# Performance work log

Measured on AMD Instinct MI355X. Metric: run time of the kernel, lower is better.

## Reference

```python
import jax, jax.numpy as jnp
import numpy as np

NBIT = 4          # weight bit-width
GROUP_SIZE = 128  # weight quantization group size (divides k)
HAS_WEIGHT_ZEROS = True


def _quant_dequant_weights(w, group_size=GROUP_SIZE, nbit=NBIT, has_zeros=HAS_WEIGHT_ZEROS):
    # Mirrors torchao _quantize + quantize_per_channel_group, then dequantizes
    # (the native kernel dequantizes inline with the matmul; math is identical).
    qmin = -(1 << (nbit - 1))
    qmax = (1 << (nbit - 1)) - 1
    n, k = w.shape
    g = w.reshape(-1, group_size)                      # [n*k/gs, gs]
    vmin = g.min(axis=1, keepdims=True)
    vmax = g.max(axis=1, keepdims=True)
    scales = (vmax - vmin) / (qmax - qmin)             # per-group scale
    if has_zeros:
        zeros = qmin - jnp.round(vmin / scales)
    else:
        zeros = jnp.zeros_like(scales)
    q = jnp.clip(jnp.round(g / scales) + zeros, qmin, qmax)
    deq = (q - zeros) * scales
    return deq.reshape(n, k)


def _dyn_quant_dequant_act(x):
    # Dynamic per-token (per-row) asymmetric int8 activation quantization.
    qmin, qmax = -128, 127
    xmin = x.min(axis=-1, keepdims=True)
    xmax = x.max(axis=-1, keepdims=True)
    scale = (xmax - xmin) / (qmax - qmin)
    zero = qmin - jnp.round(xmin / scale)
    q = jnp.clip(jnp.round(x / scale) + zero, qmin, qmax)
    return (q - zero) * scale


def setup_inputs() -> dict:
    key = jax.random.key(0)
    k1, k2 = jax.random.split(key)
    x = jax.random.normal(k1, (4, 2048, 4096), dtype=jnp.float32)
    weights = jax.random.normal(k2, (4096, 4096), dtype=jnp.float32) * 0.02
    return {"x": x, "weights": weights}


def reference(x, weights):
    w_deq = _quant_dequant_weights(weights)            # [n, k]
    x_deq = _dyn_quant_dequant_act(x)                  # [..., m, k]
    # y[..., m, n] = x_deq @ w_deq^T
    return jnp.einsum('bmk,nk->bmn', x_deq, w_deq)
```

## Files before the change

kernel.cpp:

```cpp
#include <hip/hip_runtime.h>
#include <hip/hip_bf16.h>
#include <cfloat>

typedef __attribute__((ext_vector_type(8))) short bf16x8;
typedef __attribute__((ext_vector_type(4))) float f32x4;

#define M_DIM 8192
#define N_DIM 4096
#define K_DIM 4096

__device__ inline ushort f2bf(float f) {
    unsigned u = __float_as_uint(f);
    unsigned r = (u + 0x7FFFu + ((u >> 16) & 1u)) >> 16;
    return (ushort)r;
}

#define SWZ(x) ((x) ^ ((((x) >> 7) & 7) << 4))

__global__ __launch_bounds__(256) void w_dequant(const float* __restrict__ w,
                                                 ushort* __restrict__ wq) {
    int g = blockIdx.x * 4 + (threadIdx.x >> 6);
    int lane = threadIdx.x & 63;
    const float* src = w + (size_t)g * 128;
    float2 v = *(const float2*)(src + lane * 2);
    float mn = fminf(v.x, v.y), mx = fmaxf(v.x, v.y);
#pragma unroll
    for (int s = 1; s < 64; s <<= 1) {
        mn = fminf(mn, __shfl_xor(mn, s));
        mx = fmaxf(mx, __shfl_xor(mx, s));
    }
    float scale = (mx - mn) / 15.0f;
    float zero  = -8.0f - rintf(mn / scale);
    float q0 = fminf(fmaxf(rintf(v.x / scale) + zero, -8.0f), 7.0f);
    float q1 = fminf(fmaxf(rintf(v.y / scale) + zero, -8.0f), 7.0f);
    ushort2 o;
    o.x = f2bf((q0 - zero) * scale);
    o.y = f2bf((q1 - zero) * scale);
    *(ushort2*)(wq + (size_t)g * 128 + lane * 2) = o;
}

__global__ __launch_bounds__(256) void act_qdq(const float* __restrict__ x,
                                               ushort* __restrict__ xq) {
    __shared__ float smn[4], smx[4];
    int row = blockIdx.x;
    const float* xr = x + (size_t)row * K_DIM;
    ushort* xo = xq + (size_t)row * K_DIM;
    int t = threadIdx.x;
    float4 v[4];
    float mn = FLT_MAX, mx = -FLT_MAX;
#pragma unroll
    for (int i = 0; i < 4; i++) {
        v[i] = ((const float4*)xr)[t + i * 256];
        mn = fminf(mn, fminf(fminf(v[i].x, v[i].y), fminf(v[i].z, v[i].w)));
        mx = fmaxf(mx, fmaxf(fmaxf(v[i].x, v[i].y), fmaxf(v[i].z, v[i].w)));
    }
#pragma unroll
    for (int s = 1; s < 64; s <<= 1) {
        mn = fminf(mn, __shfl_xor(mn, s));
        mx = fmaxf(mx, __shfl_xor(mx, s));
    }
    int w = t >> 6;
    if ((t & 63) == 0) { smn[w] = mn; smx[w] = mx; }
    __syncthreads();
    mn = fminf(fminf(smn[0], smn[1]), fminf(smn[2], smn[3]));
    mx = fmaxf(fmaxf(smx[0], smx[1]), fmaxf(smx[2], smx[3]));
    float scale = (mx - mn) / 255.0f;
    float zero  = -128.0f - rintf(mn / scale);
#pragma unroll
    for (int i = 0; i < 4; i++) {
        float e0 = v[i].x, e1 = v[i].y, e2 = v[i].z, e3 = v[i].w;
        ushort4 o;
        float q;
        q = fminf(fmaxf(rintf(e0 / scale) + zero, -128.0f), 127.0f); o.x = f2bf((q - zero) * scale);
        q = fminf(fmaxf(rintf(e1 / scale) + zero, -128.0f), 127.0f); o.y = f2bf((q - zero) * scale);
        q = fminf(fmaxf(rintf(e2 / scale) + zero, -128.0f), 127.0f); o.z = f2bf((q - zero) * scale);
        q = fminf(fmaxf(rintf(e3 / scale) + zero, -128.0f), 127.0f); o.w = f2bf((q - zero) * scale);
        ((ushort4*)xo)[t + i * 256] = o;
    }
}

#define BM 256
#define BN 256
#define BK 64
#define NT (K_DIM / BK)

__global__ __launch_bounds__(512, 1) void gemm_bt8(const ushort* __restrict__ A,
                                                   const ushort* __restrict__ B,
                                                   float* __restrict__ C) {
    __shared__ __align__(16) ushort As[2][BM * BK];
    __shared__ __align__(16) ushort Bs[2][BN * BK];

    const int nbx = N_DIM / BN;
    const int nwg = (M_DIM / BM) * nbx;
    int bid = blockIdx.x;
    bid = (bid & 7) * (nwg / 8) + (bid >> 3);
    int mb = bid / nbx, nb = bid % nbx;
    size_t m0 = (size_t)mb * BM, n0 = (size_t)nb * BN;

    const int t = threadIdx.x;
    const int w = t >> 6, lane = t & 63;
    const int wm = w >> 2, wn = w & 3;
    const int lr = lane & 15;
    const int lk = (lane >> 4) << 3;

    const ushort* Ab = A + m0 * K_DIM;
    const ushort* Bb = B + n0 * K_DIM;

    auto STAGE = [&](int T, int qq) {
        if (T >= NT) return;
        int d = T & 1;
        bool isA = qq < 4;
        int rq = isA ? qq : qq - 4;
        ushort* reg = isA ? As[d] : Bs[d];
        const ushort* gbase = isA ? Ab : Bb;
        int base = rq * 8192 + w * 1024;
        int lb = base + lane * 16;
        int lg = SWZ(lb);
        int r = lg >> 7;
        int c = (lg & 127) >> 1;
        __builtin_amdgcn_global_load_lds(
            (const __attribute__((address_space(1))) unsigned int*)(gbase + (size_t)r * K_DIM + T * BK + c),
            (__attribute__((address_space(3))) unsigned int*)((char*)reg + base),
            16, 0, 0);
    };

    f32x4 acc[8][4] = {};
    bf16x8 afr[2][2][2];
    bf16x8 bfr[2][4][2];

#define LOADA(S, d, q) do {                                                       \
    _Pragma("unroll") for (int ii = 0; ii < 2; ii++)                              \
    _Pragma("unroll") for (int kk = 0; kk < 2; kk++) {                            \
        int row = (q) * 64 + wm * 32 + ii * 16 + lr;                              \
        int lg = row * 128 + (kk * 32 + lk) * 2;                                  \
        afr[S][ii][kk] = *(const bf16x8*)((const char*)As[d] + SWZ(lg));          \
    } } while (0)
#define LOADB(S, d) do {                                                          \
    _Pragma("unroll") for (int ni = 0; ni < 4; ni++)                              \
    _Pragma("unroll") for (int kk = 0; kk < 2; kk++) {                            \
        int row = wn * 64 + ni * 16 + lr;                                         \
        int lg = row * 128 + (kk * 32 + lk) * 2;                                  \
        bfr[S][ni][kk] = *(const bf16x8*)((const char*)Bs[d] + SWZ(lg));          \
    } } while (0)

#define PHASE(q, SA, SB, SN, dn, qn, sT1, sq1, sT2, sq2, vm) do {                 \
    __builtin_amdgcn_s_setprio(1);                                                \
    _Pragma("unroll") for (int kk = 0; kk < 2; kk++)                              \
    _Pragma("unroll") for (int ii = 0; ii < 2; ii++)                              \
    _Pragma("unroll") for (int ni = 0; ni < 4; ni++)                              \
        acc[(q) * 2 + ii][ni] = __builtin_amdgcn_mfma_f32_16x16x32_bf16(          \
            afr[SA][ii][kk], bfr[SB][ni][kk], acc[(q) * 2 + ii][ni], 0, 0, 0);    \
    __builtin_amdgcn_s_setprio(0);                                                \
    if ((qn) == 0) LOADB(dn, dn);                                                 \
    LOADA(SN, dn, qn);                                                            \
    STAGE(sT1, sq1);                                                              \
    STAGE(sT2, sq2);                                                              \
    asm volatile("s_waitcnt lgkmcnt(0)" ::: "memory");                            \
    if ((vm) == 0) asm volatile("s_waitcnt vmcnt(6)" ::: "memory");               \
    if ((vm) == 1) asm volatile("s_waitcnt vmcnt(2)" ::: "memory");               \
    if ((vm) == 2) asm volatile("s_waitcnt vmcnt(0)" ::: "memory");               \
    __builtin_amdgcn_s_barrier();                                                 \
    __builtin_amdgcn_sched_barrier(0);                                            \
  } while (0)

    STAGE(0, 0); STAGE(0, 1); STAGE(0, 2); STAGE(0, 3);
    STAGE(0, 4); STAGE(0, 5); STAGE(0, 6); STAGE(0, 7);
    STAGE(1, 4); STAGE(1, 5); STAGE(1, 6); STAGE(1, 7);
    STAGE(1, 0); STAGE(1, 1);
    asm volatile("s_waitcnt vmcnt(6)" ::: "memory");
    __builtin_amdgcn_s_barrier();
    LOADB(0, 0);
    LOADA(0, 0, 0);
    asm volatile("s_waitcnt lgkmcnt(0)" ::: "memory");
    __builtin_amdgcn_sched_barrier(0);

#pragma unroll 1
    for (int i = 0; i < NT / 2 - 1; i++) {
        int T0 = 2 * i;
        PHASE(0, 0, 0, 1, 0, 1, T0 + 1, 2, T0 + 1, 3, 0);
        PHASE(1, 1, 0, 0, 0, 2, T0 + 2, 4, T0 + 2, 5, 0);
        PHASE(2, 0, 0, 1, 0, 3, T0 + 2, 6, T0 + 2, 7, 0);
        PHASE(3, 1, 0, 0, 1, 0, T0 + 2, 0, T0 + 2, 1, 0);
        PHASE(0, 0, 1, 1, 1, 1, T0 + 2, 2, T0 + 2, 3, 0);
        PHASE(1, 1, 1, 0, 1, 2, T0 + 3, 4, T0 + 3, 5, 0);
        PHASE(2, 0, 1, 1, 1, 3, T0 + 3, 6, T0 + 3, 7, 0);
        PHASE(3, 1, 1, 0, 0, 0, T0 + 3, 0, T0 + 3, 1, 0);
    }

    PHASE(0, 0, 0, 1, 0, 1, NT - 1, 2, NT - 1, 3, 0);
    PHASE(1, 1, 0, 0, 0, 2, NT, 0, NT, 0, 1);
    PHASE(2, 0, 0, 1, 0, 3, NT, 0, NT, 0, 2);
    PHASE(3, 1, 0, 0, 1, 0, NT, 0, NT, 0, 3);
    PHASE(0, 0, 1, 1, 1, 1, NT, 0, NT, 0, 3);
    PHASE(1, 1, 1, 0, 1, 2, NT, 0, NT, 0, 3);
    PHASE(2, 0, 1, 1, 1, 3, NT, 0, NT, 0, 3);
    PHASE(3, 1, 1, 0, 0, 0, NT, 0, NT, 0, 3);
#undef PHASE
#undef LOADA
#undef LOADB

    int fq = lane >> 4;
#pragma unroll
    for (int mi = 0; mi < 8; mi++) {
#pragma unroll
        for (int ni = 0; ni < 4; ni++) {
#pragma unroll
            for (int r = 0; r < 4; r++) {
                size_t crow = m0 + (mi >> 1) * 64 + wm * 32 + (mi & 1) * 16 + fq * 4 + r;
                C[crow * N_DIM + n0 + wn * 64 + ni * 16 + lr] = acc[mi][ni][r];
            }
        }
    }
}

extern "C" void kernel_launch(void* const* d_in, const int* in_sizes, int n_in,
                              void* d_out, int out_size, void* d_ws, size_t ws_size,
                              hipStream_t stream) {
    const float* x = (const float*)d_in[0];
    const float* w = (const float*)d_in[1];
    float* out = (float*)d_out;

    ushort* wq = (ushort*)d_ws;
    ushort* xq = (ushort*)((char*)d_ws + (size_t)N_DIM * K_DIM * 2);

    hipLaunchKernelGGL(w_dequant, dim3((N_DIM * K_DIM / 128) / 4), dim3(256), 0, stream, w, wq);
    hipLaunchKernelGGL(act_qdq, dim3(M_DIM), dim3(256), 0, stream, x, xq);
    hipLaunchKernelGGL(gemm_bt8, dim3((M_DIM / BM) * (N_DIM / BN)), dim3(512), 0, stream, xq, wq, out);
}
```

Before: 324.3 us.

## Restructure GEMM main loop into 4 half-tile phases with precomputed staging offsets

Replaces the 8-phase-per-two-tiles schedule (each phase doing 8 MFMAs on a 64-row quarter) with 4 phases that each do 32 MFMAs on a 128-row half, loading 4 A fragments at once. Global-to-LDS staging is reordered so the next tile's loads are issued earlier, with different vmcnt thresholds. Per-thread staging offsets are precomputed once instead of recomputing swizzled addresses for every load. The intent is to cut barrier count and address arithmetic per K tile. The cost is more VGPRs for A fragments and a reworked wait scheme whose correctness depends on the new load ordering.

```diff
diff --git a/kernel.cpp b/kernel.cpp
--- a/kernel.cpp
+++ b/kernel.cpp
@@ -106,98 +106,128 @@
     const ushort* Ab = A + m0 * K_DIM;
     const ushort* Bb = B + n0 * K_DIM;
 
-    auto STAGE = [&](int T, int qq) {
-        if (T >= NT) return;
-        int d = T & 1;
-        bool isA = qq < 4;
-        int rq = isA ? qq : qq - 4;
-        ushort* reg = isA ? As[d] : Bs[d];
-        const ushort* gbase = isA ? Ab : Bb;
+    int off_q[4];
+    int dst_q[4];
+#pragma unroll
+    for (int rq = 0; rq < 4; rq++) {
         int base = rq * 8192 + w * 1024;
         int lb = base + lane * 16;
         int lg = SWZ(lb);
-        int r = lg >> 7;
-        int c = (lg & 127) >> 1;
-        __builtin_amdgcn_global_load_lds(
-            (const __attribute__((address_space(1))) unsigned int*)(gbase + (size_t)r * K_DIM + T * BK + c),
-            (__attribute__((address_space(3))) unsigned int*)((char*)reg + base),
-            16, 0, 0);
-    };
+        off_q[rq] = (lg >> 7) * K_DIM + ((lg & 127) >> 1);
+        dst_q[rq] = base;
+    }
+
+#define STAGE(T, qq) do {                                                         \
+    int _d = (T) & 1;                                                             \
+    const ushort* _g = ((qq) < 4 ? Ab : Bb);                                      \
+    ushort* _l = ((qq) < 4 ? As[_d] : Bs[_d]);                                    \
+    int _rq = (qq) & 3;                                                           \
+    __builtin_amdgcn_global_load_lds(                                             \
+        (const __attribute__((address_space(1))) unsigned int*)(_g + (size_t)off_q[_rq] + (T) * BK), \
+        (__attribute__((address_space(3))) unsigned int*)((char*)_l + dst_q[_rq]),\
+        16, 0, 0);                                                                \
+  } while (0)
 
     f32x4 acc[8][4] = {};
-    bf16x8 afr[2][2][2];
+    bf16x8 afr[4][2];
     bf16x8 bfr[2][4][2];
 
-#define LOADA(S, d, q) do {                                                       \
-    _Pragma("unroll") for (int ii = 0; ii < 2; ii++)                              \
+#define LOADA(h, d) do {                                                          \
+    _Pragma("unroll") for (int mf = 0; mf < 4; mf++)                              \
     _Pragma("unroll") for (int kk = 0; kk < 2; kk++) {                            \
-        int row = (q) * 64 + wm * 32 + ii * 16 + lr;                              \
+        int row = (h) * 128 + (mf >> 1) * 64 + wm * 32 + (mf & 1) * 16 + lr;      \
         int lg = row * 128 + (kk * 32 + lk) * 2;                                  \
-        afr[S][ii][kk] = *(const bf16x8*)((const char*)As[d] + SWZ(lg));          \
+        afr[mf][kk] = *(const bf16x8*)((const char*)As[d] + SWZ(lg));             \
     } } while (0)
-#define LOADB(S, d) do {                                                          \
+#define LOADB(d) do {                                                             \
     _Pragma("unroll") for (int ni = 0; ni < 4; ni++)                              \
     _Pragma("unroll") for (int kk = 0; kk < 2; kk++) {                            \
         int row = wn * 64 + ni * 16 + lr;                                         \
         int lg = row * 128 + (kk * 32 + lk) * 2;                                  \
-        bfr[S][ni][kk] = *(const bf16x8*)((const char*)Bs[d] + SWZ(lg));          \
+        bfr[d][ni][kk] = *(const bf16x8*)((const char*)Bs[d] + SWZ(lg));          \
     } } while (0)
 
-#define PHASE(q, SA, SB, SN, dn, qn, sT1, sq1, sT2, sq2, vm) do {                 \
+#define BAR1() do {                                                               \
+    __builtin_amdgcn_s_barrier();                                                 \
+    asm volatile("s_waitcnt lgkmcnt(0)" ::: "memory");                            \
+    __builtin_amdgcn_sched_barrier(0);                                            \
+  } while (0)
+
+#define MFMA_PH(h, dB) do {                                                       \
     __builtin_amdgcn_s_setprio(1);                                                \
     _Pragma("unroll") for (int kk = 0; kk < 2; kk++)                              \
-    _Pragma("unroll") for (int ii = 0; ii < 2; ii++)                              \
+    _Pragma("unroll") for (int mf = 0; mf < 4; mf++)                              \
     _Pragma("unroll") for (int ni = 0; ni < 4; ni++)                              \
-        acc[(q) * 2 + ii][ni] = __builtin_amdgcn_mfma_f32_16x16x32_bf16(          \
-            afr[SA][ii][kk], bfr[SB][ni][kk], acc[(q) * 2 + ii][ni], 0, 0, 0);    \
+        acc[(h) * 4 + mf][ni] = __builtin_amdgcn_mfma_f32_16x16x32_bf16(          \
+            afr[mf][kk], bfr[dB][ni][kk], acc[(h) * 4 + mf][ni], 0, 0, 0);        \
     __builtin_amdgcn_s_setprio(0);                                                \
-    if ((qn) == 0) LOADB(dn, dn);                                                 \
-    LOADA(SN, dn, qn);                                                            \
-    STAGE(sT1, sq1);                                                              \
-    STAGE(sT2, sq2);                                                              \
-    asm volatile("s_waitcnt lgkmcnt(0)" ::: "memory");                            \
-    if ((vm) == 0) asm volatile("s_waitcnt vmcnt(6)" ::: "memory");               \
-    if ((vm) == 1) asm volatile("s_waitcnt vmcnt(2)" ::: "memory");               \
-    if ((vm) == 2) asm volatile("s_waitcnt vmcnt(0)" ::: "memory");               \
+  } while (0)
+
+#define ENDPH(vm) do {                                                            \
+    asm volatile("s_waitcnt " vm ::: "memory");                                   \
     __builtin_amdgcn_s_barrier();                                                 \
     __builtin_amdgcn_sched_barrier(0);                                            \
   } while (0)
 
     STAGE(0, 0); STAGE(0, 1); STAGE(0, 2); STAGE(0, 3);
     STAGE(0, 4); STAGE(0, 5); STAGE(0, 6); STAGE(0, 7);
-    STAGE(1, 4); STAGE(1, 5); STAGE(1, 6); STAGE(1, 7);
-    STAGE(1, 0); STAGE(1, 1);
-    asm volatile("s_waitcnt vmcnt(6)" ::: "memory");
+    STAGE(1, 4); STAGE(1, 5); STAGE(1, 6); STAGE(1, 7); STAGE(1, 0); STAGE(1, 1);
+    STAGE(1, 2); STAGE(1, 3);
+    asm volatile("s_waitcnt vmcnt(8)" ::: "memory");
     __builtin_amdgcn_s_barrier();
-    LOADB(0, 0);
-    LOADA(0, 0, 0);
+    LOADB(0);
+
+#pragma unroll 1
+    for (int i = 0; i < NT / 2 - 1; i++) {
+        int E = 2 * i, O = 2 * i + 1;
+        LOADA(0, 0);
+        STAGE(E + 2, 0); STAGE(E + 2, 1); STAGE(E + 2, 4); STAGE(E + 2, 5);
+        BAR1();
+        MFMA_PH(0, 0);
+        ENDPH("vmcnt(6)");
+        LOADA(1, 0);
+        LOADB(1);
+        STAGE(E + 2, 6); STAGE(E + 2, 7); STAGE(E + 2, 2); STAGE(E + 2, 3);
+        BAR1();
+        MFMA_PH(1, 0);
+        ENDPH("vmcnt(8)");
+        LOADA(0, 1);
+        STAGE(O + 2, 4); STAGE(O + 2, 5); STAGE(O + 2, 6); STAGE(O + 2, 7);
+        STAGE(O + 2, 0); STAGE(O + 2, 1);
+        BAR1();
+        MFMA_PH(0, 1);
+        ENDPH("vmcnt(6)");
+        LOADA(1, 1);
+        LOADB(0);
+        STAGE(O + 2, 2); STAGE(O + 2, 3);
+        BAR1();
+        MFMA_PH(1, 1);
+        ENDPH("vmcnt(8)");
+    }
+
+    LOADA(0, 0);
+    BAR1();
+    MFMA_PH(0, 0);
+    ENDPH("vmcnt(2)");
+    LOADA(1, 0);
+    LOADB(1);
+    BAR1();
+    MFMA_PH(1, 0);
+    ENDPH("vmcnt(0)");
+    LOADA(0, 1);
     asm volatile("s_waitcnt lgkmcnt(0)" ::: "memory");
     __builtin_amdgcn_sched_barrier(0);
-
-#pragma unroll 1
-    for (int i = 0; i < NT / 2 - 1; i++) {
-        int T0 = 2 * i;
-        PHASE(0, 0, 0, 1, 0, 1, T0 + 1, 2, T0 + 1, 3, 0);
-        PHASE(1, 1, 0, 0, 0, 2, T0 + 2, 4, T0 + 2, 5, 0);
-        PHASE(2, 0, 0, 1, 0, 3, T0 + 2, 6, T0 + 2, 7, 0);
-        PHASE(3, 1, 0, 0, 1, 0, T0 + 2, 0, T0 + 2, 1, 0);
-        PHASE(0, 0, 1, 1, 1, 1, T0 + 2, 2, T0 + 2, 3, 0);
-        PHASE(1, 1, 1, 0, 1, 2, T0 + 3, 4, T0 + 3, 5, 0);
-        PHASE(2, 0, 1, 1, 1, 3, T0 + 3, 6, T0 + 3, 7, 0);
-        PHASE(3, 1, 1, 0, 0, 0, T0 + 3, 0, T0 + 3, 1, 0);
-    }
-
-    PHASE(0, 0, 0, 1, 0, 1, NT - 1, 2, NT - 1, 3, 0);
-    PHASE(1, 1, 0, 0, 0, 2, NT, 0, NT, 0, 1);
-    PHASE(2, 0, 0, 1, 0, 3, NT, 0, NT, 0, 2);
-    PHASE(3, 1, 0, 0, 1, 0, NT, 0, NT, 0, 3);
-    PHASE(0, 0, 1, 1, 1, 1, NT, 0, NT, 0, 3);
-    PHASE(1, 1, 1, 0, 1, 2, NT, 0, NT, 0, 3);
-    PHASE(2, 0, 1, 1, 1, 3, NT, 0, NT, 0, 3);
-    PHASE(3, 1, 1, 0, 0, 0, NT, 0, NT, 0, 3);
-#undef PHASE
+    MFMA_PH(0, 1);
+    LOADA(1, 1);
+    asm volatile("s_waitcnt lgkmcnt(0)" ::: "memory");
+    __builtin_amdgcn_sched_barrier(0);
+    MFMA_PH(1, 1);
+#undef STAGE
 #undef LOADA
 #undef LOADB
+#undef BAR1
+#undef MFMA_PH
+#undef ENDPH
 
     int fq = lane >> 4;
 #pragma unroll
```

Result: slower. 788.5 us (+143.2%).

## Pack dequantized weights in MFMA fragment order and load B directly to registers

Applied to the files above, without the earlier changes.

The weight dequant kernel now writes bf16 weights pre-permuted into the per-wave MFMA fragment layout. The GEMM then reads B fragments straight from global memory into registers, dropping the B shared-memory tile and its staging. The pipeline becomes a simpler two-buffer A-only LDS scheme, and the block-to-tile mapping is changed so each XCD covers a set of M rows. This cuts LDS traffic and frees LDS, but B now comes from global or L2 with less latency hiding, and the deep phased schedule is replaced by a coarser one.

```diff
diff --git a/kernel.cpp b/kernel.cpp
--- a/kernel.cpp
+++ b/kernel.cpp
@@ -17,26 +17,43 @@
 
 #define SWZ(x) ((x) ^ ((((x) >> 7) & 7) << 4))
 
-__global__ __launch_bounds__(256) void w_dequant(const float* __restrict__ w,
+__global__ __launch_bounds__(256) void w_dq_pack(const float* __restrict__ w,
                                                  ushort* __restrict__ wq) {
-    int g = blockIdx.x * 4 + (threadIdx.x >> 6);
-    int lane = threadIdx.x & 63;
-    const float* src = w + (size_t)g * 128;
-    float2 v = *(const float2*)(src + lane * 2);
-    float mn = fminf(v.x, v.y), mx = fmaxf(v.x, v.y);
-#pragma unroll
-    for (int s = 1; s < 64; s <<= 1) {
-        mn = fminf(mn, __shfl_xor(mn, s));
-        mx = fmaxf(mx, __shfl_xor(mx, s));
-    }
+    int bx = blockIdx.x;
+    int n0 = (bx >> 5) * 64;
+    int kg = bx & 31;
+    int t = threadIdx.x;
+    int n = n0 + (t >> 2);
+    int kq = t & 3;
+    const float* src = w + (size_t)n * K_DIM + kg * 128 + kq * 32;
+    float4 v[8];
+    float mn = FLT_MAX, mx = -FLT_MAX;
+#pragma unroll
+    for (int j = 0; j < 8; j++) {
+        v[j] = ((const float4*)src)[j];
+        mn = fminf(mn, fminf(fminf(v[j].x, v[j].y), fminf(v[j].z, v[j].w)));
+        mx = fmaxf(mx, fmaxf(fmaxf(v[j].x, v[j].y), fmaxf(v[j].z, v[j].w)));
+    }
+    mn = fminf(mn, __shfl_xor(mn, 1)); mx = fmaxf(mx, __shfl_xor(mx, 1));
+    mn = fminf(mn, __shfl_xor(mn, 2)); mx = fmaxf(mx, __shfl_xor(mx, 2));
     float scale = (mx - mn) / 15.0f;
     float zero  = -8.0f - rintf(mn / scale);
-    float q0 = fminf(fmaxf(rintf(v.x / scale) + zero, -8.0f), 7.0f);
-    float q1 = fminf(fmaxf(rintf(v.y / scale) + zero, -8.0f), 7.0f);
-    ushort2 o;
-    o.x = f2bf((q0 - zero) * scale);
-    o.y = f2bf((q1 - zero) * scale);
-    *(ushort2*)(wq + (size_t)g * 128 + lane * 2) = o;
+
+    int nb = n >> 8, wn = (n >> 6) & 3, ni = (n >> 4) & 3, lr = n & 15;
+    int T = kg * 2 + (kq >> 1), kk = kq & 1;
+    size_t base16 = ((((size_t)(nb * 4 + wn) * 64 + T) * 2 + kk) * 4 + ni) * 64;
+#pragma unroll
+    for (int lh = 0; lh < 4; lh++) {
+        bf16x8 o;
+#pragma unroll
+        for (int e = 0; e < 8; e++) {
+            float4 vv = v[lh * 2 + (e >> 2)];
+            float x = (e & 3) == 0 ? vv.x : (e & 3) == 1 ? vv.y : (e & 3) == 2 ? vv.z : vv.w;
+            float q = fminf(fmaxf(rintf(x / scale) + zero, -8.0f), 7.0f);
+            o[e] = (short)f2bf((q - zero) * scale);
+        }
+        *(bf16x8*)(wq + (base16 + lh * 16 + lr) * 8) = o;
+    }
 }
 
 __global__ __launch_bounds__(256) void act_qdq(const float* __restrict__ x,
@@ -68,13 +85,12 @@
     float zero  = -128.0f - rintf(mn / scale);
 #pragma unroll
     for (int i = 0; i < 4; i++) {
-        float e0 = v[i].x, e1 = v[i].y, e2 = v[i].z, e3 = v[i].w;
         ushort4 o;
         float q;
-        q = fminf(fmaxf(rintf(e0 / scale) + zero, -128.0f), 127.0f); o.x = f2bf((q - zero) * scale);
-        q = fminf(fmaxf(rintf(e1 / scale) + zero, -128.0f), 127.0f); o.y = f2bf((q - zero) * scale);
-        q = fminf(fmaxf(rintf(e2 / scale) + zero, -128.0f), 127.0f); o.z = f2bf((q - zero) * scale);
-        q = fminf(fmaxf(rintf(e3 / scale) + zero, -128.0f), 127.0f); o.w = f2bf((q - zero) * scale);
+        q = fminf(fmaxf(rintf(v[i].x / scale) + zero, -128.0f), 127.0f); o.x = f2bf((q - zero) * scale);
+        q = fminf(fmaxf(rintf(v[i].y / scale) + zero, -128.0f), 127.0f); o.y = f2bf((q - zero) * scale);
+        q = fminf(fmaxf(rintf(v[i].z / scale) + zero, -128.0f), 127.0f); o.z = f2bf((q - zero) * scale);
+        q = fminf(fmaxf(rintf(v[i].w / scale) + zero, -128.0f), 127.0f); o.w = f2bf((q - zero) * scale);
         ((ushort4*)xo)[t + i * 256] = o;
     }
 }
@@ -85,17 +101,15 @@
 #define NT (K_DIM / BK)
 
 __global__ __launch_bounds__(512, 1) void gemm_bt8(const ushort* __restrict__ A,
-                                                   const ushort* __restrict__ B,
+                                                   const ushort* __restrict__ Bp,
                                                    float* __restrict__ C) {
     __shared__ __align__(16) ushort As[2][BM * BK];
-    __shared__ __align__(16) ushort Bs[2][BN * BK];
-
-    const int nbx = N_DIM / BN;
-    const int nwg = (M_DIM / BM) * nbx;
-    int bid = blockIdx.x;
-    bid = (bid & 7) * (nwg / 8) + (bid >> 3);
-    int mb = bid / nbx, nb = bid % nbx;
-    size_t m0 = (size_t)mb * BM, n0 = (size_t)nb * BN;
+
+    int orig = blockIdx.x;
+    int xcd = orig & 7, j = orig >> 3;
+    int mb = xcd * 4 + (j & 3);
+    int nb = j >> 2;
+    size_t m0 = (size_t)mb * BM;
 
     const int t = threadIdx.x;
     const int w = t >> 6, lane = t & 63;
@@ -104,101 +118,83 @@
     const int lk = (lane >> 4) << 3;
 
     const ushort* Ab = A + m0 * K_DIM;
-    const ushort* Bb = B + n0 * K_DIM;
-
-    auto STAGE = [&](int T, int qq) {
-        if (T >= NT) return;
-        int d = T & 1;
-        bool isA = qq < 4;
-        int rq = isA ? qq : qq - 4;
-        ushort* reg = isA ? As[d] : Bs[d];
-        const ushort* gbase = isA ? Ab : Bb;
-        int base = rq * 8192 + w * 1024;
-        int lb = base + lane * 16;
-        int lg = SWZ(lb);
-        int r = lg >> 7;
-        int c = (lg & 127) >> 1;
-        __builtin_amdgcn_global_load_lds(
-            (const __attribute__((address_space(1))) unsigned int*)(gbase + (size_t)r * K_DIM + T * BK + c),
-            (__attribute__((address_space(3))) unsigned int*)((char*)reg + base),
-            16, 0, 0);
-    };
+    const ushort* Bpk = Bp + (size_t)(nb * 4 + wn) * 64 * 4096;
 
     f32x4 acc[8][4] = {};
-    bf16x8 afr[2][2][2];
+    bf16x8 afr[4][2];
     bf16x8 bfr[2][4][2];
 
-#define LOADA(S, d, q) do {                                                       \
-    _Pragma("unroll") for (int ii = 0; ii < 2; ii++)                              \
+#define STAGEALL(dd, T) do {                                                      \
+    _Pragma("unroll") for (int rq = 0; rq < 4; rq++) {                            \
+        int base = rq * 8192 + w * 1024;                                          \
+        int lb = base + lane * 16;                                                \
+        int lg = SWZ(lb);                                                         \
+        __builtin_amdgcn_global_load_lds(                                         \
+            (const __attribute__((address_space(1))) unsigned int*)(Ab + (size_t)(lg >> 7) * K_DIM + (T) * BK + ((lg & 127) >> 1)), \
+            (__attribute__((address_space(3))) unsigned int*)((char*)As[dd] + base), \
+            16, 0, 0);                                                            \
+    } } while (0)
+
+#define LOADA_H(h, dd) do {                                                       \
+    _Pragma("unroll") for (int mf = 0; mf < 4; mf++)                              \
     _Pragma("unroll") for (int kk = 0; kk < 2; kk++) {                            \
-        int row = (q) * 64 + wm * 32 + ii * 16 + lr;                              \
+        int mi = (h) * 4 + mf;                                                    \
+        int row = (mi >> 1) * 64 + wm * 32 + (mi & 1) * 16 + lr;                  \
         int lg = row * 128 + (kk * 32 + lk) * 2;                                  \
-        afr[S][ii][kk] = *(const bf16x8*)((const char*)As[d] + SWZ(lg));          \
+        afr[mf][kk] = *(const bf16x8*)((const char*)As[dd] + SWZ(lg));            \
     } } while (0)
-#define LOADB(S, d) do {                                                          \
+
+#define LOADBG(dd, T) do {                                                        \
+    const ushort* bp = Bpk + (size_t)(T) * 4096;                                  \
+    _Pragma("unroll") for (int kk = 0; kk < 2; kk++)                              \
     _Pragma("unroll") for (int ni = 0; ni < 4; ni++)                              \
-    _Pragma("unroll") for (int kk = 0; kk < 2; kk++) {                            \
-        int row = wn * 64 + ni * 16 + lr;                                         \
-        int lg = row * 128 + (kk * 32 + lk) * 2;                                  \
-        bfr[S][ni][kk] = *(const bf16x8*)((const char*)Bs[d] + SWZ(lg));          \
-    } } while (0)
-
-#define PHASE(q, SA, SB, SN, dn, qn, sT1, sq1, sT2, sq2, vm) do {                 \
+        bfr[dd][ni][kk] = *(const bf16x8*)(bp + ((kk * 4 + ni) * 64 + lane) * 8); \
+    } while (0)
+
+#define MFMAH(h, dd) do {                                                         \
     __builtin_amdgcn_s_setprio(1);                                                \
     _Pragma("unroll") for (int kk = 0; kk < 2; kk++)                              \
-    _Pragma("unroll") for (int ii = 0; ii < 2; ii++)                              \
+    _Pragma("unroll") for (int mf = 0; mf < 4; mf++)                              \
     _Pragma("unroll") for (int ni = 0; ni < 4; ni++)                              \
-        acc[(q) * 2 + ii][ni] = __builtin_amdgcn_mfma_f32_16x16x32_bf16(          \
-            afr[SA][ii][kk], bfr[SB][ni][kk], acc[(q) * 2 + ii][ni], 0, 0, 0);    \
+        acc[(h) * 4 + mf][ni] = __builtin_amdgcn_mfma_f32_16x16x32_bf16(          \
+            afr[mf][kk], bfr[dd][ni][kk], acc[(h) * 4 + mf][ni], 0, 0, 0);        \
     __builtin_amdgcn_s_setprio(0);                                                \
-    if ((qn) == 0) LOADB(dn, dn);                                                 \
-    LOADA(SN, dn, qn);                                                            \
-    STAGE(sT1, sq1);                                                              \
-    STAGE(sT2, sq2);                                                              \
+  } while (0)
+
+#define ITER(d, T) do {                                                           \
+    if ((T) + 1 < NT) STAGEALL((d) ^ 1, (T) + 1);                                 \
+    LOADA_H(0, d);                                                                \
+    if ((T) + 1 < NT) LOADBG((d) ^ 1, (T) + 1);                                   \
     asm volatile("s_waitcnt lgkmcnt(0)" ::: "memory");                            \
-    if ((vm) == 0) asm volatile("s_waitcnt vmcnt(6)" ::: "memory");               \
-    if ((vm) == 1) asm volatile("s_waitcnt vmcnt(2)" ::: "memory");               \
-    if ((vm) == 2) asm volatile("s_waitcnt vmcnt(0)" ::: "memory");               \
+    __builtin_amdgcn_sched_barrier(0);                                            \
+    MFMAH(0, d);                                                                  \
+    LOADA_H(1, d);                                                                \
+    asm volatile("s_waitcnt lgkmcnt(0)" ::: "memory");                            \
+    __builtin_amdgcn_sched_barrier(0);                                            \
+    MFMAH(1, d);                                                                  \
+    asm volatile("s_waitcnt vmcnt(8)" ::: "memory");                              \
     __builtin_amdgcn_s_barrier();                                                 \
     __builtin_amdgcn_sched_barrier(0);                                            \
   } while (0)
 
-    STAGE(0, 0); STAGE(0, 1); STAGE(0, 2); STAGE(0, 3);
-    STAGE(0, 4); STAGE(0, 5); STAGE(0, 6); STAGE(0, 7);
-    STAGE(1, 4); STAGE(1, 5); STAGE(1, 6); STAGE(1, 7);
-    STAGE(1, 0); STAGE(1, 1);
-    asm volatile("s_waitcnt vmcnt(6)" ::: "memory");
+    STAGEALL(0, 0);
+    LOADBG(0, 0);
+    asm volatile("s_waitcnt vmcnt(0)" ::: "memory");
     __builtin_amdgcn_s_barrier();
-    LOADB(0, 0);
-    LOADA(0, 0, 0);
-    asm volatile("s_waitcnt lgkmcnt(0)" ::: "memory");
     __builtin_amdgcn_sched_barrier(0);
 
 #pragma unroll 1
-    for (int i = 0; i < NT / 2 - 1; i++) {
-        int T0 = 2 * i;
-        PHASE(0, 0, 0, 1, 0, 1, T0 + 1, 2, T0 + 1, 3, 0);
-        PHASE(1, 1, 0, 0, 0, 2, T0 + 2, 4, T0 + 2, 5, 0);
-        PHASE(2, 0, 0, 1, 0, 3, T0 + 2, 6, T0 + 2, 7, 0);
-        PHASE(3, 1, 0, 0, 1, 0, T0 + 2, 0, T0 + 2, 1, 0);
-        PHASE(0, 0, 1, 1, 1, 1, T0 + 2, 2, T0 + 2, 3, 0);
-        PHASE(1, 1, 1, 0, 1, 2, T0 + 3, 4, T0 + 3, 5, 0);
-        PHASE(2, 0, 1, 1, 1, 3, T0 + 3, 6, T0 + 3, 7, 0);
-        PHASE(3, 1, 1, 0, 0, 0, T0 + 3, 0, T0 + 3, 1, 0);
-    }
-
-    PHASE(0, 0, 0, 1, 0, 1, NT - 1, 2, NT - 1, 3, 0);
-    PHASE(1, 1, 0, 0, 0, 2, NT, 0, NT, 0, 1);
-    PHASE(2, 0, 0, 1, 0, 3, NT, 0, NT, 0, 2);
-    PHASE(3, 1, 0, 0, 1, 0, NT, 0, NT, 0, 3);
-    PHASE(0, 0, 1, 1, 1, 1, NT, 0, NT, 0, 3);
-    PHASE(1, 1, 1, 0, 1, 2, NT, 0, NT, 0, 3);
-    PHASE(2, 0, 1, 1, 1, 3, NT, 0, NT, 0, 3);
-    PHASE(3, 1, 1, 0, 0, 0, NT, 0, NT, 0, 3);
-#undef PHASE
-#undef LOADA
-#undef LOADB
-
+    for (int i = 0; i < NT / 2; i++) {
+        ITER(0, 2 * i);
+        ITER(1, 2 * i + 1);
+    }
+#undef ITER
+#undef MFMAH
+#undef LOADBG
+#undef LOADA_H
+#undef STAGEALL
+
+    size_t n0 = (size_t)nb * BN;
     int fq = lane >> 4;
 #pragma unroll
     for (int mi = 0; mi < 8; mi++) {
@@ -223,7 +219,7 @@
     ushort* wq = (ushort*)d_ws;
     ushort* xq = (ushort*)((char*)d_ws + (size_t)N_DIM * K_DIM * 2);
 
-    hipLaunchKernelGGL(w_dequant, dim3((N_DIM * K_DIM / 128) / 4), dim3(256), 0, stream, w, wq);
+    hipLaunchKernelGGL(w_dq_pack, dim3((N_DIM / 64) * (K_DIM / 128)), dim3(256), 0, stream, w, wq);
     hipLaunchKernelGGL(act_qdq, dim3(M_DIM), dim3(256), 0, stream, x, xq);
     hipLaunchKernelGGL(gemm_bt8, dim3((M_DIM / BM) * (N_DIM / BN)), dim3(512), 0, stream, xq, wq, out);
 }
```

After: 1.024 ms. +215.9%, slower.
